# Optimization experiments

Hardware: AMD Instinct MI355X
Metric: run time of the kernel (lower is better)

## Reference

```python
import jax, jax.numpy as jnp
import numpy as np

C_IN, SEQ_LEN, N_KERNELS, KSS, KS_MAX, BATCH = 1, 512, 1000, [7, 9, 11], 11, 64


def setup_inputs() -> dict:
    rng = np.random.default_rng(0)
    ks_l, dil_l, pad_l, lout_l = [], [], [], []
    W = np.zeros((N_KERNELS, C_IN, KS_MAX), dtype=np.float32)
    for k in range(N_KERNELS):
        ks = int(rng.choice(KSS))
        d_f = 2.0 ** rng.uniform(0.0, np.log2((SEQ_LEN - 1) // (ks - 1)))
        pad = int((ks - 1) * d_f // 2) if rng.integers(2) == 1 else 0
        d = int(d_f)
        # torch passes padding=2*pad to Conv1d -> adds 2*pad on EACH side
        lout = SEQ_LEN + 4 * pad - d * (ks - 1)
        w = rng.standard_normal((1, C_IN, ks)).astype(np.float32)
        w -= w.mean()  # center like the original (global mean)
        W[k, :, :ks] = w[0]
        ks_l.append(ks); dil_l.append(d); pad_l.append(pad); lout_l.append(lout)
    dils = np.asarray(dil_l, dtype=np.int64)
    pads = np.asarray(pad_l, dtype=np.int64)
    l_out = np.asarray(lout_l, dtype=np.int32)
    max_L = int(l_out.max())
    t = np.arange(max_L)
    j = np.arange(KS_MAX)
    # raw input index for output position t, tap j of kernel k
    raw = t[None, None, :] - 2 * pads[:, None, None] + j[None, :, None] * dils[:, None, None]
    valid = (raw >= 0) & (raw < SEQ_LEN)  # zero-padding semantics
    idx = np.clip(raw, 0, SEQ_LEN - 1).astype(np.int32)
    bias = (2.0 * (rng.random(N_KERNELS) - 0.5)).astype(np.float32)
    key = jax.random.key(0)
    x = jax.random.normal(key, (BATCH, C_IN, SEQ_LEN), dtype=jnp.float32)
    return {
        "x": x,
        "weight": jnp.asarray(W),
        "bias": jnp.asarray(bias),
        "idx": jnp.asarray(idx),
        "valid": jnp.asarray(valid),
        "l_out": jnp.asarray(l_out),
    }


def _forward(x, weight, bias, idx, valid, l_out):
    B = x.shape[0]
    K, C, KS = weight.shape
    L = idx.shape[-1]
    validf = valid.astype(x.dtype)  # [K, KS, L]
    acc = jnp.zeros((B, K, L), dtype=x.dtype)
    for j in range(KS):  # fixed small tap loop; each kernel vectorized over K
        xg = x[:, :, idx[:, j, :]]  # [B, C, K, L] gather along time
        acc = acc + jnp.einsum("bckt,kc->bkt", xg, weight[:, :, j]) * validf[None, :, j, :]
    out = acc + bias[None, :, None]  # [B, K, L]
    tmask = jnp.arange(L)[None, :] < l_out[:, None]  # [K, L] valid output positions
    neg = jnp.finfo(x.dtype).min
    mx = jnp.max(jnp.where(tmask[None], out, neg), axis=-1)  # [B, K]
    ppv = jnp.sum(jnp.where(tmask[None] & (out > 0), 1.0, 0.0), axis=-1) / l_out.astype(x.dtype)[None]
    # torch interleaves [max_i, ppv_i] along dim=1
    return jnp.stack([mx, ppv], axis=-1).reshape(B, 2 * K)


def reference(x, weight, bias, idx, valid, l_out):
    return _forward(x, weight, bias, idx, valid, l_out)
```

## Files before the change

### kernel.cpp

```cpp
#include <hip/hip_runtime.h>
#include <hip/hip_fp16.h>
#include <float.h>

constexpr int KMAX  = 11;
constexpr int SEQ   = 512;
constexpr int NB    = 64;
constexpr int NBB   = 8;
constexpr int NGRP  = NB / NBB;
constexpr int KPB   = 4;
constexpr int MSTR  = 32;
constexpr int SBASE = 512;
constexpr int WSLOT = 1600;

__device__ __forceinline__ unsigned h2b(__half2 h) { unsigned u; __builtin_memcpy(&u, &h, 4); return u; }
__device__ __forceinline__ __half2  b2h(unsigned u) { __half2 h; __builtin_memcpy(&h, &u, 4); return h; }

__device__ __forceinline__ unsigned pkmax(unsigned a, unsigned b) {
    unsigned d; asm("v_pk_max_f16 %0, %1, %2" : "=v"(d) : "v"(a), "v"(b)); return d;
}
__device__ __forceinline__ unsigned pkadd(unsigned a, unsigned b) { return h2b(__hadd2(b2h(a), b2h(b))); }
__device__ __forceinline__ __half2 h2max(__half2 a, __half2 b) { return b2h(pkmax(h2b(a), h2b(b))); }
__device__ __forceinline__ unsigned pkfma_clamp(unsigned a, unsigned b, unsigned c) {
    unsigned d; asm("v_pk_fma_f16 %0, %1, %2, %3 clamp" : "=v"(d) : "v"(a), "v"(b), "v"(c)); return d;
}

template<int CTRL>
__device__ __forceinline__ unsigned dppmov(unsigned old, unsigned v) {
    return (unsigned)__builtin_amdgcn_update_dpp((int)old, (int)v, CTRL, 0xF, 0xF, false);
}
constexpr unsigned NEGINF2 = 0xFC00FC00u;

__device__ __forceinline__ unsigned dpp_redmax(unsigned x) {
    x = pkmax(x, dppmov<0xB1 >(NEGINF2, x));
    x = pkmax(x, dppmov<0x4E >(NEGINF2, x));
    x = pkmax(x, dppmov<0x141>(NEGINF2, x));
    x = pkmax(x, dppmov<0x140>(NEGINF2, x));
    x = pkmax(x, dppmov<0x142>(NEGINF2, x));
    x = pkmax(x, dppmov<0x143>(NEGINF2, x));
    return x;
}
__device__ __forceinline__ unsigned dpp_redadd(unsigned x) {
    x = pkadd(x, dppmov<0xB1 >(0u, x));
    x = pkadd(x, dppmov<0x4E >(0u, x));
    x = pkadd(x, dppmov<0x141>(0u, x));
    x = pkadd(x, dppmov<0x140>(0u, x));
    x = pkadd(x, dppmov<0x142>(0u, x));
    x = pkadd(x, dppmov<0x143>(0u, x));
    return x;
}

__global__ __launch_bounds__(256)
void prep_kernel(const float* __restrict__ x, const float* __restrict__ w,
                 const int* __restrict__ idx, int* __restrict__ meta,
                 unsigned short* __restrict__ xt, int K, int maxL)
{
    const int tid = threadIdx.x;
    if ((int)blockIdx.x >= K) {
        const int j  = ((int)blockIdx.x - K) * 256 + tid;
        const int b  = j >> 7, s4 = j & 127;
        const float4 v = reinterpret_cast<const float4*>(x)[b * (SEQ / 4) + s4];
        const int g = b >> 3, bl = b & 7;
        unsigned short* dst = xt + ((size_t)g * SEQ + s4 * 4) * NBB + bl;
        __half h;
        h = __float2half_rn(v.x); __builtin_memcpy(&dst[0 * NBB], &h, 2);
        h = __float2half_rn(v.y); __builtin_memcpy(&dst[1 * NBB], &h, 2);
        h = __float2half_rn(v.z); __builtin_memcpy(&dst[2 * NBB], &h, 2);
        h = __float2half_rn(v.w); __builtin_memcpy(&dst[3 * NBB], &h, 2);
        return;
    }

    __shared__ int c_sh[KMAX];
    const int k = blockIdx.x, wave = tid >> 6, lane = tid & 63;

    for (int j = wave; j < KMAX; j += 4) {
        const int* row = idx + ((size_t)k * KMAX + j) * (size_t)maxL;
        int c = 0;
        for (int base = 0; base < maxL; base += 64) {
            const int t = base + lane;
            const int v = (t < maxL) ? row[t] : 0;
            const bool interior = (v > 0) && (v < SEQ - 1);
            const unsigned long long mb = __ballot(interior);
            if (mb != 0ull) {
                const int fl = __builtin_ctzll(mb);
                c = __shfl(v, fl) - (base + fl);
                break;
            }
        }
        if (lane == 0) c_sh[j] = c;
    }
    __syncthreads();

    if (tid == 0) {
        int* mk = meta + (size_t)k * MSTR;
        int n = 0;
        for (int j = 0; j < KMAX; ++j) {
            const float wj = w[(size_t)k * KMAX + j];
            if (wj != 0.0f) {
                mk[1 + n] = c_sh[j];
                __half hw = __float2half_rn(wj);
                unsigned short ub; __builtin_memcpy(&ub, &hw, 2);
                mk[12 + n] = (unsigned)ub | ((unsigned)ub << 16);
                ++n;
            }
        }
        for (int jj = n; jj < KMAX; ++jj) { mk[1 + jj] = 0; mk[12 + jj] = 0; }
        mk[0] = n;
    }
}

template<int NJ>
__device__ __forceinline__ void conv_wave(
    const char* __restrict__ xsc, int mrow, int lout, int lane, unsigned ctermb,
    unsigned (&um)[4], unsigned (&uc)[4])
{
    const __half2 zero2 = __float2half2_rn(0.f);
    const __half2 nbig2 = __float2half2_rn(-65504.f);
    const unsigned C4b  = 0x74007400u;

    int addr[NJ]; __half2 wr[NJ];
#pragma unroll
    for (int j = 0; j < NJ; ++j) {
        const int c = __builtin_amdgcn_readlane(mrow, 1 + j);
        wr[j]   = b2h((unsigned)__builtin_amdgcn_readlane(mrow, 12 + j));
        addr[j] = (lane + c + SBASE) * 16;
    }
    __half2 mx2[4], ct2[4];
#pragma unroll
    for (int m = 0; m < 4; ++m) { mx2[m] = nbig2; ct2[m] = zero2; }

    const int nfull = lout >> 6;
    const int ng4   = nfull >> 2;

    for (int g = 0; g < ng4; ++g) {
#pragma unroll
        for (int u = 0; u < 4; ++u) {
            uint4 d[NJ];
#pragma unroll
            for (int j = 0; j < NJ; ++j)
                d[j] = *reinterpret_cast<const uint4*>(xsc + addr[j] + u * 1024);
            __half2 a[4] = {zero2, zero2, zero2, zero2};
#pragma unroll
            for (int j = 0; j < NJ; ++j) {
                a[0] = __hfma2(wr[j], b2h(d[j].x), a[0]);
                a[1] = __hfma2(wr[j], b2h(d[j].y), a[1]);
                a[2] = __hfma2(wr[j], b2h(d[j].z), a[2]);
                a[3] = __hfma2(wr[j], b2h(d[j].w), a[3]);
            }
#pragma unroll
            for (int m = 0; m < 4; ++m) {
                mx2[m] = h2max(mx2[m], a[m]);
                ct2[m] = b2h(pkadd(h2b(ct2[m]), pkfma_clamp(h2b(a[m]), C4b, ctermb)));
            }
        }
#pragma unroll
        for (int j = 0; j < NJ; ++j) addr[j] += 4096;
    }
    for (int u = 0; u < (nfull & 3); ++u) {
        uint4 d[NJ];
#pragma unroll
        for (int j = 0; j < NJ; ++j)
            d[j] = *reinterpret_cast<const uint4*>(xsc + addr[j]);
        __half2 a[4] = {zero2, zero2, zero2, zero2};
#pragma unroll
        for (int j = 0; j < NJ; ++j) {
            a[0] = __hfma2(wr[j], b2h(d[j].x), a[0]);
            a[1] = __hfma2(wr[j], b2h(d[j].y), a[1]);
            a[2] = __hfma2(wr[j], b2h(d[j].z), a[2]);
            a[3] = __hfma2(wr[j], b2h(d[j].w), a[3]);
        }
#pragma unroll
        for (int m = 0; m < 4; ++m) {
            mx2[m] = h2max(mx2[m], a[m]);
            ct2[m] = b2h(pkadd(h2b(ct2[m]), pkfma_clamp(h2b(a[m]), C4b, ctermb)));
        }
#pragma unroll
        for (int j = 0; j < NJ; ++j) addr[j] += 1024;
    }
    const int rem = lout & 63;
    if (rem) {
        uint4 d[NJ];
#pragma unroll
        for (int j = 0; j < NJ; ++j)
            d[j] = *reinterpret_cast<const uint4*>(xsc + addr[j]);
        __half2 a[4] = {zero2, zero2, zero2, zero2};
#pragma unroll
        for (int j = 0; j < NJ; ++j) {
            a[0] = __hfma2(wr[j], b2h(d[j].x), a[0]);
            a[1] = __hfma2(wr[j], b2h(d[j].y), a[1]);
            a[2] = __hfma2(wr[j], b2h(d[j].z), a[2]);
            a[3] = __hfma2(wr[j], b2h(d[j].w), a[3]);
        }
        const bool tm = lane < rem;
#pragma unroll
        for (int m = 0; m < 4; ++m) {
            a[m] = tm ? a[m] : nbig2;
            mx2[m] = h2max(mx2[m], a[m]);
            ct2[m] = b2h(pkadd(h2b(ct2[m]), pkfma_clamp(h2b(a[m]), C4b, ctermb)));
        }
    }

#pragma unroll
    for (int m = 0; m < 4; ++m) {
        um[m] = dpp_redmax(h2b(mx2[m]));
        uc[m] = dpp_redadd(h2b(ct2[m]));
    }
}

__global__ __launch_bounds__(256, 4)
void rocket_main(const unsigned short* __restrict__ xt, const int* __restrict__ meta,
                 const float* __restrict__ bias, const int* __restrict__ l_out,
                 float* __restrict__ out, int K)
{
    __shared__ __align__(16) unsigned xs_u[WSLOT * 4];

    const int kbase = (int)blockIdx.x * KPB;
    const int grp   = blockIdx.y;
    const int tid   = threadIdx.x;
    const int wave  = tid >> 6, lane = tid & 63;

    float4* xs4 = reinterpret_cast<float4*>(xs_u);
    const float4* src = reinterpret_cast<const float4*>(xt + (size_t)grp * SEQ * NBB);
    const float4 z4 = make_float4(0.f, 0.f, 0.f, 0.f);
    for (int i = tid; i < WSLOT; i += 256) {
        const int s = i - SBASE;
        xs4[i] = ((unsigned)s < (unsigned)SEQ) ? src[s] : z4;
    }
    __syncthreads();

    const int k = kbase + wave;
    if (k >= K) return;

    const int mrow  = meta[(size_t)k * MSTR + (lane & 31)];
    const int nj    = __builtin_amdgcn_readlane(mrow, 0);
    const int lout  = __builtin_amdgcn_readfirstlane(l_out[k]);
    const float biasf = __int_as_float(__builtin_amdgcn_readfirstlane(__float_as_int(bias[k])));
    const unsigned ctermb = h2b(__float2half2_rn(biasf * 16384.f));

    unsigned um[4], uc[4];
    const char* xsc = reinterpret_cast<const char*>(xs_u);
    if (nj <= 7)      conv_wave<7 >(xsc, mrow, lout, lane, ctermb, um, uc);
    else if (nj <= 9) conv_wave<9 >(xsc, mrow, lout, lane, ctermb, um, uc);
    else              conv_wave<11>(xsc, mrow, lout, lane, ctermb, um, uc);

    if (lane == 63) {
        const float loutf = (float)lout;
#pragma unroll
        for (int m = 0; m < 4; ++m) {
            const __half2 hm = b2h(um[m]);
            const __half2 hc = b2h(uc[m]);
            float* o0 = out + (size_t)(grp * NBB + 2 * m) * (2 * K) + 2 * k;
            o0[0] = __low2float(hm) + biasf;
            o0[1] = __low2float(hc) / loutf;
            float* o1 = o0 + 2 * K;
            o1[0] = __high2float(hm) + biasf;
            o1[1] = __high2float(hc) / loutf;
        }
    }
}

extern "C" void kernel_launch(void* const* d_in, const int* in_sizes, int n_in,
                              void* d_out, int out_size, void* d_ws, size_t ws_size,
                              hipStream_t stream)
{
    const float* x    = (const float*)d_in[0];
    const float* w    = (const float*)d_in[1];
    const float* bias = (const float*)d_in[2];
    const int*   idx  = (const int*)d_in[3];
    const int*   lout = (const int*)d_in[5];
    float* out = (float*)d_out;

    const int K    = in_sizes[2];
    const int maxL = in_sizes[3] / (K * KMAX);

    int* meta = (int*)d_ws;
    size_t meta_bytes = ((size_t)K * MSTR * sizeof(int) + 255) & ~(size_t)255;
    unsigned short* xt = (unsigned short*)((char*)d_ws + meta_bytes);

    prep_kernel<<<K + 32, 256, 0, stream>>>(x, w, idx, meta, xt, K, maxL);
    rocket_main<<<dim3((K + KPB - 1) / KPB, NGRP), 256, 0, stream>>>(xt, meta, bias, lout, out, K);
}
```

Baseline: 31.21 us.

## Split conv tap loads between LDS and padded global buffer; sparse idx probe

The time-major half-precision input buffer is now stored in global memory with zero padding that matches the LDS window layout, filled by extra prep blocks. The convolution loop then reads odd taps from global memory (through the cache) and even taps from LDS, spreading load bandwidth across both paths. The prep kernel also finds each tap's offset by sampling every 16th index first and falls back to a full scan only if that fails. The cost is extra global traffic and higher latency on half the loads, plus additional prep blocks for the padding writes.

```diff
diff --git a/kernel.cpp b/kernel.cpp
--- a/kernel.cpp
+++ b/kernel.cpp
@@ -11,6 +11,8 @@
 constexpr int MSTR  = 32;
 constexpr int SBASE = 512;
 constexpr int WSLOT = 1600;
+constexpr int NPAD  = NGRP * (WSLOT - SEQ);
+constexpr int ZBLK  = (NPAD + 255) / 256;
 
 __device__ __forceinline__ unsigned h2b(__half2 h) { unsigned u; __builtin_memcpy(&u, &h, 4); return u; }
 __device__ __forceinline__ __half2  b2h(unsigned u) { __half2 h; __builtin_memcpy(&h, &u, 4); return h; }
@@ -52,15 +54,27 @@
 __global__ __launch_bounds__(256)
 void prep_kernel(const float* __restrict__ x, const float* __restrict__ w,
                  const int* __restrict__ idx, int* __restrict__ meta,
-                 unsigned short* __restrict__ xt, int K, int maxL)
+                 unsigned short* __restrict__ xtg, int K, int maxL)
 {
     const int tid = threadIdx.x;
-    if ((int)blockIdx.x >= K) {
-        const int j  = ((int)blockIdx.x - K) * 256 + tid;
+    const int blk = blockIdx.x;
+    if (blk >= K + 32) {
+        const int p = (blk - K - 32) * 256 + tid;
+        if (p < NPAD) {
+            const int g = p / (WSLOT - SEQ);
+            const int r = p - g * (WSLOT - SEQ);
+            const int slot = (r < SBASE) ? r : r + SEQ;
+            *reinterpret_cast<float4*>(xtg + ((size_t)g * WSLOT + slot) * NBB) =
+                make_float4(0.f, 0.f, 0.f, 0.f);
+        }
+        return;
+    }
+    if (blk >= K) {
+        const int j  = (blk - K) * 256 + tid;
         const int b  = j >> 7, s4 = j & 127;
         const float4 v = reinterpret_cast<const float4*>(x)[b * (SEQ / 4) + s4];
         const int g = b >> 3, bl = b & 7;
-        unsigned short* dst = xt + ((size_t)g * SEQ + s4 * 4) * NBB + bl;
+        unsigned short* dst = xtg + ((size_t)g * WSLOT + SBASE + s4 * 4) * NBB + bl;
         __half h;
         h = __float2half_rn(v.x); __builtin_memcpy(&dst[0 * NBB], &h, 2);
         h = __float2half_rn(v.y); __builtin_memcpy(&dst[1 * NBB], &h, 2);
@@ -70,23 +84,41 @@
     }
 
     __shared__ int c_sh[KMAX];
-    const int k = blockIdx.x, wave = tid >> 6, lane = tid & 63;
-
-    for (int j = wave; j < KMAX; j += 4) {
-        const int* row = idx + ((size_t)k * KMAX + j) * (size_t)maxL;
-        int c = 0;
-        for (int base = 0; base < maxL; base += 64) {
-            const int t = base + lane;
-            const int v = (t < maxL) ? row[t] : 0;
-            const bool interior = (v > 0) && (v < SEQ - 1);
+    const int k = blk, wave = tid >> 6, lane = tid & 63;
+    const int tprobe = min(lane * 16, maxL - 1);
+
+    int vv[3] = {0, 0, 0};
+#pragma unroll
+    for (int i = 0; i < 3; ++i) {
+        const int j = wave + i * 4;
+        if (j < KMAX) vv[i] = idx[((size_t)k * KMAX + j) * (size_t)maxL + tprobe];
+    }
+#pragma unroll
+    for (int i = 0; i < 3; ++i) {
+        const int j = wave + i * 4;
+        if (j < KMAX) {
+            int c = 0;
+            const bool interior = (vv[i] > 0) && (vv[i] < SEQ - 1);
             const unsigned long long mb = __ballot(interior);
             if (mb != 0ull) {
                 const int fl = __builtin_ctzll(mb);
-                c = __shfl(v, fl) - (base + fl);
-                break;
-            }
-        }
-        if (lane == 0) c_sh[j] = c;
+                c = __shfl(vv[i], fl) - min(fl * 16, maxL - 1);
+            } else {
+                const int* row = idx + ((size_t)k * KMAX + j) * (size_t)maxL;
+                for (int base = 0; base < maxL; base += 64) {
+                    const int t2 = base + lane;
+                    const int v2 = (t2 < maxL) ? row[t2] : 0;
+                    const bool in2 = (v2 > 0) && (v2 < SEQ - 1);
+                    const unsigned long long mb2 = __ballot(in2);
+                    if (mb2 != 0ull) {
+                        const int fl2 = __builtin_ctzll(mb2);
+                        c = __shfl(v2, fl2) - (base + fl2);
+                        break;
+                    }
+                }
+            }
+            if (lane == 0) c_sh[j] = c;
+        }
     }
     __syncthreads();
 
@@ -110,7 +142,8 @@
 
 template<int NJ>
 __device__ __forceinline__ void conv_wave(
-    const char* __restrict__ xsc, int mrow, int lout, int lane, unsigned ctermb,
+    const char* __restrict__ xsc, const char* __restrict__ gxt,
+    int mrow, int lout, int lane, unsigned ctermb,
     unsigned (&um)[4], unsigned (&uc)[4])
 {
     const __half2 zero2 = __float2half2_rn(0.f);
@@ -136,8 +169,10 @@
         for (int u = 0; u < 4; ++u) {
             uint4 d[NJ];
 #pragma unroll
-            for (int j = 0; j < NJ; ++j)
-                d[j] = *reinterpret_cast<const uint4*>(xsc + addr[j] + u * 1024);
+            for (int j = 0; j < NJ; ++j) {
+                if (j & 1) d[j] = *reinterpret_cast<const uint4*>(gxt + addr[j] + u * 1024);
+                else       d[j] = *reinterpret_cast<const uint4*>(xsc + addr[j] + u * 1024);
+            }
             __half2 a[4] = {zero2, zero2, zero2, zero2};
 #pragma unroll
             for (int j = 0; j < NJ; ++j) {
@@ -158,8 +193,10 @@
     for (int u = 0; u < (nfull & 3); ++u) {
         uint4 d[NJ];
 #pragma unroll
-        for (int j = 0; j < NJ; ++j)
-            d[j] = *reinterpret_cast<const uint4*>(xsc + addr[j]);
+        for (int j = 0; j < NJ; ++j) {
+            if (j & 1) d[j] = *reinterpret_cast<const uint4*>(gxt + addr[j]);
+            else       d[j] = *reinterpret_cast<const uint4*>(xsc + addr[j]);
+        }
         __half2 a[4] = {zero2, zero2, zero2, zero2};
 #pragma unroll
         for (int j = 0; j < NJ; ++j) {
@@ -180,8 +217,10 @@
     if (rem) {
         uint4 d[NJ];
 #pragma unroll
-        for (int j = 0; j < NJ; ++j)
-            d[j] = *reinterpret_cast<const uint4*>(xsc + addr[j]);
+        for (int j = 0; j < NJ; ++j) {
+            if (j & 1) d[j] = *reinterpret_cast<const uint4*>(gxt + addr[j]);
+            else       d[j] = *reinterpret_cast<const uint4*>(xsc + addr[j]);
+        }
         __half2 a[4] = {zero2, zero2, zero2, zero2};
 #pragma unroll
         for (int j = 0; j < NJ; ++j) {
@@ -207,7 +246,7 @@
 }
 
 __global__ __launch_bounds__(256, 4)
-void rocket_main(const unsigned short* __restrict__ xt, const int* __restrict__ meta,
+void rocket_main(const unsigned short* __restrict__ xtg, const int* __restrict__ meta,
                  const float* __restrict__ bias, const int* __restrict__ l_out,
                  float* __restrict__ out, int K)
 {
@@ -219,7 +258,7 @@
     const int wave  = tid >> 6, lane = tid & 63;
 
     float4* xs4 = reinterpret_cast<float4*>(xs_u);
-    const float4* src = reinterpret_cast<const float4*>(xt + (size_t)grp * SEQ * NBB);
+    const float4* src = reinterpret_cast<const float4*>(xtg) + (size_t)grp * WSLOT + SBASE;
     const float4 z4 = make_float4(0.f, 0.f, 0.f, 0.f);
     for (int i = tid; i < WSLOT; i += 256) {
         const int s = i - SBASE;
@@ -238,9 +277,10 @@
 
     unsigned um[4], uc[4];
     const char* xsc = reinterpret_cast<const char*>(xs_u);
-    if (nj <= 7)      conv_wave<7 >(xsc, mrow, lout, lane, ctermb, um, uc);
-    else if (nj <= 9) conv_wave<9 >(xsc, mrow, lout, lane, ctermb, um, uc);
-    else              conv_wave<11>(xsc, mrow, lout, lane, ctermb, um, uc);
+    const char* gxt = reinterpret_cast<const char*>(xtg) + (size_t)grp * WSLOT * 16;
+    if (nj <= 7)      conv_wave<7 >(xsc, gxt, mrow, lout, lane, ctermb, um, uc);
+    else if (nj <= 9) conv_wave<9 >(xsc, gxt, mrow, lout, lane, ctermb, um, uc);
+    else              conv_wave<11>(xsc, gxt, mrow, lout, lane, ctermb, um, uc);
 
     if (lane == 63) {
         const float loutf = (float)lout;
@@ -274,8 +314,8 @@
 
     int* meta = (int*)d_ws;
     size_t meta_bytes = ((size_t)K * MSTR * sizeof(int) + 255) & ~(size_t)255;
-    unsigned short* xt = (unsigned short*)((char*)d_ws + meta_bytes);
-
-    prep_kernel<<<K + 32, 256, 0, stream>>>(x, w, idx, meta, xt, K, maxL);
-    rocket_main<<<dim3((K + KPB - 1) / KPB, NGRP), 256, 0, stream>>>(xt, meta, bias, lout, out, K);
-}
+    unsigned short* xtg = (unsigned short*)((char*)d_ws + meta_bytes);
+
+    prep_kernel<<<K + 32 + ZBLK, 256, 0, stream>>>(x, w, idx, meta, xtg, K, maxL);
+    rocket_main<<<dim3((K + KPB - 1) / KPB, NGRP), 256, 0, stream>>>(xtg, meta, bias, lout, out, K);
+}
```

After: 41.13 us. 1.32x slower.

## Shrink shared-memory halo and skip taps whose 64-lane window lies in padding

Applied to the files above, without the earlier changes.

The input tile in LDS shrinks from a 1600-slot zero-padded window to 640 slots with a 64-slot halo on each side. Each tap's load and FMA is skipped when its whole 64-lane window falls outside the real signal, so zero-padding reads and multiplies are avoided. Unused taps get a huge offset so they are always skipped. The smaller LDS footprint allows launch bounds of 8 blocks per CU, and the per-kernel offset probe now samples strided indices once before falling back to a scan. The cost is a per-tap branch in the inner loop, and correctness depends on partially padded windows staying within the 64-slot halo.

```diff
diff --git a/kernel.cpp b/kernel.cpp
--- a/kernel.cpp
+++ b/kernel.cpp
@@ -9,8 +9,8 @@
 constexpr int NGRP  = NB / NBB;
 constexpr int KPB   = 4;
 constexpr int MSTR  = 32;
-constexpr int SBASE = 512;
-constexpr int WSLOT = 1600;
+constexpr int X0    = 64;
+constexpr int WSLOT = 640;
 
 __device__ __forceinline__ unsigned h2b(__half2 h) { unsigned u; __builtin_memcpy(&u, &h, 4); return u; }
 __device__ __forceinline__ __half2  b2h(unsigned u) { __half2 h; __builtin_memcpy(&h, &u, 4); return h; }
@@ -71,22 +71,40 @@
 
     __shared__ int c_sh[KMAX];
     const int k = blockIdx.x, wave = tid >> 6, lane = tid & 63;
-
-    for (int j = wave; j < KMAX; j += 4) {
-        const int* row = idx + ((size_t)k * KMAX + j) * (size_t)maxL;
-        int c = 0;
-        for (int base = 0; base < maxL; base += 64) {
-            const int t = base + lane;
-            const int v = (t < maxL) ? row[t] : 0;
-            const bool interior = (v > 0) && (v < SEQ - 1);
+    const int tprobe = min(lane * 16, maxL - 1);
+
+    int vv[3] = {0, 0, 0};
+#pragma unroll
+    for (int i = 0; i < 3; ++i) {
+        const int j = wave + i * 4;
+        if (j < KMAX) vv[i] = idx[((size_t)k * KMAX + j) * (size_t)maxL + tprobe];
+    }
+#pragma unroll
+    for (int i = 0; i < 3; ++i) {
+        const int j = wave + i * 4;
+        if (j < KMAX) {
+            int c = 0;
+            const bool interior = (vv[i] > 0) && (vv[i] < SEQ - 1);
             const unsigned long long mb = __ballot(interior);
             if (mb != 0ull) {
                 const int fl = __builtin_ctzll(mb);
-                c = __shfl(v, fl) - (base + fl);
-                break;
-            }
-        }
-        if (lane == 0) c_sh[j] = c;
+                c = __shfl(vv[i], fl) - min(fl * 16, maxL - 1);
+            } else {
+                const int* row = idx + ((size_t)k * KMAX + j) * (size_t)maxL;
+                for (int base = 0; base < maxL; base += 64) {
+                    const int t2 = base + lane;
+                    const int v2 = (t2 < maxL) ? row[t2] : 0;
+                    const bool in2 = (v2 > 0) && (v2 < SEQ - 1);
+                    const unsigned long long mb2 = __ballot(in2);
+                    if (mb2 != 0ull) {
+                        const int fl2 = __builtin_ctzll(mb2);
+                        c = __shfl(v2, fl2) - (base + fl2);
+                        break;
+                    }
+                }
+            }
+            if (lane == 0) c_sh[j] = c;
+        }
     }
     __syncthreads();
 
@@ -103,7 +121,7 @@
                 ++n;
             }
         }
-        for (int jj = n; jj < KMAX; ++jj) { mk[1 + jj] = 0; mk[12 + jj] = 0; }
+        for (int jj = n; jj < KMAX; ++jj) { mk[1 + jj] = 1 << 20; mk[12 + jj] = 0; }
         mk[0] = n;
     }
 }
@@ -117,12 +135,12 @@
     const __half2 nbig2 = __float2half2_rn(-65504.f);
     const unsigned C4b  = 0x74007400u;
 
-    int addr[NJ]; __half2 wr[NJ];
+    int addr[NJ], cs[NJ]; __half2 wr[NJ];
 #pragma unroll
     for (int j = 0; j < NJ; ++j) {
-        const int c = __builtin_amdgcn_readlane(mrow, 1 + j);
+        cs[j]   = __builtin_amdgcn_readlane(mrow, 1 + j);
         wr[j]   = b2h((unsigned)__builtin_amdgcn_readlane(mrow, 12 + j));
-        addr[j] = (lane + c + SBASE) * 16;
+        addr[j] = (lane + cs[j] + X0) * 16;
     }
     __half2 mx2[4], ct2[4];
 #pragma unroll
@@ -132,19 +150,20 @@
     const int ng4   = nfull >> 2;
 
     for (int g = 0; g < ng4; ++g) {
+        const int gb = g * 256;
 #pragma unroll
         for (int u = 0; u < 4; ++u) {
-            uint4 d[NJ];
-#pragma unroll
-            for (int j = 0; j < NJ; ++j)
-                d[j] = *reinterpret_cast<const uint4*>(xsc + addr[j] + u * 1024);
+            const int tb = gb + u * 64;
             __half2 a[4] = {zero2, zero2, zero2, zero2};
 #pragma unroll
             for (int j = 0; j < NJ; ++j) {
-                a[0] = __hfma2(wr[j], b2h(d[j].x), a[0]);
-                a[1] = __hfma2(wr[j], b2h(d[j].y), a[1]);
-                a[2] = __hfma2(wr[j], b2h(d[j].z), a[2]);
-                a[3] = __hfma2(wr[j], b2h(d[j].w), a[3]);
+                if ((unsigned)(tb + cs[j] + 63) < 575u) {
+                    const uint4 d = *reinterpret_cast<const uint4*>(xsc + addr[j] + u * 1024);
+                    a[0] = __hfma2(wr[j], b2h(d.x), a[0]);
+                    a[1] = __hfma2(wr[j], b2h(d.y), a[1]);
+                    a[2] = __hfma2(wr[j], b2h(d.z), a[2]);
+                    a[3] = __hfma2(wr[j], b2h(d.w), a[3]);
+                }
             }
 #pragma unroll
             for (int m = 0; m < 4; ++m) {
@@ -156,17 +175,17 @@
         for (int j = 0; j < NJ; ++j) addr[j] += 4096;
     }
     for (int u = 0; u < (nfull & 3); ++u) {
-        uint4 d[NJ];
-#pragma unroll
-        for (int j = 0; j < NJ; ++j)
-            d[j] = *reinterpret_cast<const uint4*>(xsc + addr[j]);
+        const int tb = ng4 * 256 + u * 64;
         __half2 a[4] = {zero2, zero2, zero2, zero2};
 #pragma unroll
         for (int j = 0; j < NJ; ++j) {
-            a[0] = __hfma2(wr[j], b2h(d[j].x), a[0]);
-            a[1] = __hfma2(wr[j], b2h(d[j].y), a[1]);
-            a[2] = __hfma2(wr[j], b2h(d[j].z), a[2]);
-            a[3] = __hfma2(wr[j], b2h(d[j].w), a[3]);
+            if ((unsigned)(tb + cs[j] + 63) < 575u) {
+                const uint4 d = *reinterpret_cast<const uint4*>(xsc + addr[j]);
+                a[0] = __hfma2(wr[j], b2h(d.x), a[0]);
+                a[1] = __hfma2(wr[j], b2h(d.y), a[1]);
+                a[2] = __hfma2(wr[j], b2h(d.z), a[2]);
+                a[3] = __hfma2(wr[j], b2h(d.w), a[3]);
+            }
         }
 #pragma unroll
         for (int m = 0; m < 4; ++m) {
@@ -178,17 +197,17 @@
     }
     const int rem = lout & 63;
     if (rem) {
-        uint4 d[NJ];
-#pragma unroll
-        for (int j = 0; j < NJ; ++j)
-            d[j] = *reinterpret_cast<const uint4*>(xsc + addr[j]);
+        const int tb = nfull * 64;
         __half2 a[4] = {zero2, zero2, zero2, zero2};
 #pragma unroll
         for (int j = 0; j < NJ; ++j) {
-            a[0] = __hfma2(wr[j], b2h(d[j].x), a[0]);
-            a[1] = __hfma2(wr[j], b2h(d[j].y), a[1]);
-            a[2] = __hfma2(wr[j], b2h(d[j].z), a[2]);
-            a[3] = __hfma2(wr[j], b2h(d[j].w), a[3]);
+            if ((unsigned)(tb + cs[j] + 63) < 575u) {
+                const uint4 d = *reinterpret_cast<const uint4*>(xsc + addr[j]);
+                a[0] = __hfma2(wr[j], b2h(d.x), a[0]);
+                a[1] = __hfma2(wr[j], b2h(d.y), a[1]);
+                a[2] = __hfma2(wr[j], b2h(d.z), a[2]);
+                a[3] = __hfma2(wr[j], b2h(d.w), a[3]);
+            }
         }
         const bool tm = lane < rem;
 #pragma unroll
@@ -206,7 +225,7 @@
     }
 }
 
-__global__ __launch_bounds__(256, 4)
+__global__ __launch_bounds__(256, 8)
 void rocket_main(const unsigned short* __restrict__ xt, const int* __restrict__ meta,
                  const float* __restrict__ bias, const int* __restrict__ l_out,
                  float* __restrict__ out, int K)
@@ -219,12 +238,13 @@
     const int wave  = tid >> 6, lane = tid & 63;
 
     float4* xs4 = reinterpret_cast<float4*>(xs_u);
+    if (tid < 2 * X0) {
+        const int slot = (tid < X0) ? tid : tid + SEQ;
+        xs4[slot] = make_float4(0.f, 0.f, 0.f, 0.f);
+    }
     const float4* src = reinterpret_cast<const float4*>(xt + (size_t)grp * SEQ * NBB);
-    const float4 z4 = make_float4(0.f, 0.f, 0.f, 0.f);
-    for (int i = tid; i < WSLOT; i += 256) {
-        const int s = i - SBASE;
-        xs4[i] = ((unsigned)s < (unsigned)SEQ) ? src[s] : z4;
-    }
+    xs4[X0 + tid]       = src[tid];
+    xs4[X0 + 256 + tid] = src[256 + tid];
     __syncthreads();
 
     const int k = kbase + wave;
```

After: 34.48 us. 10.5% more time.

## Process eight kernels per block and probe idx offsets with strided single-load ballot

Applied to the files above, without the earlier changes.

The conv kernel now handles eight filters per block: each wave loops over two filters, so the staged shared-memory input tile is reused across more filters and fewer blocks repeat the global-to-LDS load. The metadata pass now finds each tap's index offset with one strided load per lane (every 16th position) and a ballot. It falls back to the old sequential 64-wide scan only when that probe finds no interior index. This trades fewer blocks, and so less parallelism, for less staging traffic and shorter serial scans in the prep kernel.

```diff
diff --git a/kernel.cpp b/kernel.cpp
--- a/kernel.cpp
+++ b/kernel.cpp
@@ -7,7 +7,7 @@
 constexpr int NB    = 64;
 constexpr int NBB   = 8;
 constexpr int NGRP  = NB / NBB;
-constexpr int KPB   = 4;
+constexpr int KPB   = 8;
 constexpr int MSTR  = 32;
 constexpr int SBASE = 512;
 constexpr int WSLOT = 1600;
@@ -71,22 +71,40 @@
 
     __shared__ int c_sh[KMAX];
     const int k = blockIdx.x, wave = tid >> 6, lane = tid & 63;
-
-    for (int j = wave; j < KMAX; j += 4) {
-        const int* row = idx + ((size_t)k * KMAX + j) * (size_t)maxL;
-        int c = 0;
-        for (int base = 0; base < maxL; base += 64) {
-            const int t = base + lane;
-            const int v = (t < maxL) ? row[t] : 0;
-            const bool interior = (v > 0) && (v < SEQ - 1);
+    const int tprobe = min(lane * 16, maxL - 1);
+
+    int vv[3] = {0, 0, 0};
+#pragma unroll
+    for (int i = 0; i < 3; ++i) {
+        const int j = wave + i * 4;
+        if (j < KMAX) vv[i] = idx[((size_t)k * KMAX + j) * (size_t)maxL + tprobe];
+    }
+#pragma unroll
+    for (int i = 0; i < 3; ++i) {
+        const int j = wave + i * 4;
+        if (j < KMAX) {
+            int c = 0;
+            const bool interior = (vv[i] > 0) && (vv[i] < SEQ - 1);
             const unsigned long long mb = __ballot(interior);
             if (mb != 0ull) {
                 const int fl = __builtin_ctzll(mb);
-                c = __shfl(v, fl) - (base + fl);
-                break;
-            }
-        }
-        if (lane == 0) c_sh[j] = c;
+                c = __shfl(vv[i], fl) - min(fl * 16, maxL - 1);
+            } else {
+                const int* row = idx + ((size_t)k * KMAX + j) * (size_t)maxL;
+                for (int base = 0; base < maxL; base += 64) {
+                    const int t2 = base + lane;
+                    const int v2 = (t2 < maxL) ? row[t2] : 0;
+                    const bool in2 = (v2 > 0) && (v2 < SEQ - 1);
+                    const unsigned long long mb2 = __ballot(in2);
+                    if (mb2 != 0ull) {
+                        const int fl2 = __builtin_ctzll(mb2);
+                        c = __shfl(v2, fl2) - (base + fl2);
+                        break;
+                    }
+                }
+            }
+            if (lane == 0) c_sh[j] = c;
+        }
     }
     __syncthreads();
 
@@ -227,33 +245,37 @@
     }
     __syncthreads();
 
-    const int k = kbase + wave;
-    if (k >= K) return;
-
-    const int mrow  = meta[(size_t)k * MSTR + (lane & 31)];
-    const int nj    = __builtin_amdgcn_readlane(mrow, 0);
-    const int lout  = __builtin_amdgcn_readfirstlane(l_out[k]);
-    const float biasf = __int_as_float(__builtin_amdgcn_readfirstlane(__float_as_int(bias[k])));
-    const unsigned ctermb = h2b(__float2half2_rn(biasf * 16384.f));
-
-    unsigned um[4], uc[4];
     const char* xsc = reinterpret_cast<const char*>(xs_u);
-    if (nj <= 7)      conv_wave<7 >(xsc, mrow, lout, lane, ctermb, um, uc);
-    else if (nj <= 9) conv_wave<9 >(xsc, mrow, lout, lane, ctermb, um, uc);
-    else              conv_wave<11>(xsc, mrow, lout, lane, ctermb, um, uc);
-
-    if (lane == 63) {
-        const float loutf = (float)lout;
-#pragma unroll
-        for (int m = 0; m < 4; ++m) {
-            const __half2 hm = b2h(um[m]);
-            const __half2 hc = b2h(uc[m]);
-            float* o0 = out + (size_t)(grp * NBB + 2 * m) * (2 * K) + 2 * k;
-            o0[0] = __low2float(hm) + biasf;
-            o0[1] = __low2float(hc) / loutf;
-            float* o1 = o0 + 2 * K;
-            o1[0] = __high2float(hm) + biasf;
-            o1[1] = __high2float(hc) / loutf;
+
+#pragma unroll 1
+    for (int r = 0; r < KPB / 4; ++r) {
+        const int k = kbase + r * 4 + wave;
+        if (k >= K) continue;
+
+        const int mrow  = meta[(size_t)k * MSTR + (lane & 31)];
+        const int nj    = __builtin_amdgcn_readlane(mrow, 0);
+        const int lout  = __builtin_amdgcn_readfirstlane(l_out[k]);
+        const float biasf = __int_as_float(__builtin_amdgcn_readfirstlane(__float_as_int(bias[k])));
+        const unsigned ctermb = h2b(__float2half2_rn(biasf * 16384.f));
+
+        unsigned um[4], uc[4];
+        if (nj <= 7)      conv_wave<7 >(xsc, mrow, lout, lane, ctermb, um, uc);
+        else if (nj <= 9) conv_wave<9 >(xsc, mrow, lout, lane, ctermb, um, uc);
+        else              conv_wave<11>(xsc, mrow, lout, lane, ctermb, um, uc);
+
+        if (lane == 63) {
+            const float loutf = (float)lout;
+#pragma unroll
+            for (int m = 0; m < 4; ++m) {
+                const __half2 hm = b2h(um[m]);
+                const __half2 hc = b2h(uc[m]);
+                float* o0 = out + (size_t)(grp * NBB + 2 * m) * (2 * K) + 2 * k;
+                o0[0] = __low2float(hm) + biasf;
+                o0[1] = __low2float(hc) / loutf;
+                float* o1 = o0 + 2 * K;
+                o1[0] = __high2float(hm) + biasf;
+                o1[1] = __high2float(hc) / loutf;
+            }
         }
     }
 }
```

Result: slower. 38.61 us (+23.7%).
